# Kernel tuning notes

Measured on AMD Instinct MI355X. Metric: run time of the kernel, lower is better.

The kernel has to match this reference:

```python
import jax, jax.numpy as jnp
import numpy as np

B, S, N, C, D = 1, 6, 10000, 128, 4
HEADS, PTS = 4, 8
HF, WF = 28, 50
M = HF * WF


def setup_inputs() -> dict:
    key0 = jax.random.key(0)
    ks = jax.random.split(key0, 14)
    sc = C ** -0.5
    d = {}
    d["query"] = jax.random.normal(ks[0], (B, N, C), jnp.float32)
    d["key"] = jax.random.normal(ks[1], (S, M, B, C), jnp.float32)
    d["value"] = jax.random.normal(ks[2], (S, M, B, C), jnp.float32)
    d["query_pos"] = jax.random.normal(ks[3], (B, N, C), jnp.float32) * 0.1
    d["reference_points_cam"] = jax.random.uniform(ks[4], (S, B, N, D, 2), jnp.float32, -0.2, 1.2)
    d["bev_mask"] = jax.random.randint(ks[5], (S, B, N, D), 0, 2).astype(bool)
    d["w_off"] = jax.random.normal(ks[6], (C, HEADS * PTS * 2), jnp.float32) * sc
    d["b_off"] = jax.random.normal(ks[7], (HEADS * PTS * 2,), jnp.float32) * 0.01
    d["w_attn"] = jax.random.normal(ks[8], (C, HEADS * PTS), jnp.float32) * sc
    d["b_attn"] = jax.random.normal(ks[9], (HEADS * PTS,), jnp.float32) * 0.01
    d["w_val"] = jax.random.normal(ks[10], (C, C), jnp.float32) * sc
    d["b_val"] = jax.random.normal(ks[11], (C,), jnp.float32) * 0.01
    d["w_out"] = jax.random.normal(ks[12], (C, C), jnp.float32) * sc
    d["b_out"] = jax.random.normal(ks[13], (C,), jnp.float32) * 0.01
    d["Hf"] = HF
    d["Wf"] = WF
    return d


def reference(query, key, value, query_pos, reference_points_cam, bev_mask,
              w_off, b_off, w_attn, b_attn, w_val, b_val, w_out, b_out, Hf, Wf):
    # SpatialCrossAttention with MSDeformAttn3D (BEVFormer semantics, eval mode: dropout=identity).
    # The torch data-dependent gather/rebatch/scatter is replaced by mathematically equivalent
    # masked computation: deformable attention is per-query independent, so running it for all
    # BEV queries per camera and mask-accumulating yields identical slots.
    B_, N_, C_ = query.shape
    S_ = key.shape[0]
    D_ = reference_points_cam.shape[3]
    H, P = HEADS, PTS
    dh = C_ // H
    Pd = P // D_
    q = query + query_pos  # (B,N,C)
    off = (q @ w_off + b_off).reshape(B_, N_, H, Pd, D_, 2)
    aw = jax.nn.softmax((q @ w_attn + b_attn).reshape(B_, N_, H, P), axis=-1)  # over levels*points (L=1)
    # value projection; per-camera feature maps laid out as (B,S,H,Hf*Wf,dh)
    v = jnp.transpose(value, (2, 0, 1, 3))  # (B,S,M,C)
    v = v @ w_val + b_val
    v = v.reshape(B_, S_, Hf * Wf, H, dh).transpose(0, 1, 3, 2, 4)  # (B,S,H,M,dh)
    ref = jnp.transpose(reference_points_cam, (1, 0, 2, 3, 4))  # (B,S,N,D,2)
    norm = jnp.array([Wf, Hf], jnp.float32)  # offset_normalizer = (W, H)
    loc = ref[:, :, :, None, None, :, :] + off[:, None] / norm  # (B,S,N,H,Pd,D,2)
    loc = loc.reshape(B_, S_, N_, H, P, 2)
    # bilinear sampling, zero padding, align_corners=False
    ix = loc[..., 0] * Wf - 0.5
    iy = loc[..., 1] * Hf - 0.5
    x0 = jnp.floor(ix)
    y0 = jnp.floor(iy)

    def flat(a):  # (B,S,N,H,P) -> (B,S,H,N*P)
        return a.transpose(0, 1, 3, 2, 4).reshape(B_, S_, H, N_ * P)

    def gather(xi, yi):
        ok = (xi >= 0) & (xi < Wf) & (yi >= 0) & (yi < Hf)
        xi_c = jnp.clip(xi, 0, Wf - 1).astype(jnp.int32)
        yi_c = jnp.clip(yi, 0, Hf - 1).astype(jnp.int32)
        idx = flat(yi_c * Wf + xi_c)
        g = jnp.take_along_axis(v, idx[..., None], axis=3)  # (B,S,H,N*P,dh)
        return g * flat(ok.astype(v.dtype))[..., None]

    wx1 = ix - x0
    wy1 = iy - y0
    wx0 = 1.0 - wx1
    wy0 = 1.0 - wy1
    samp = (gather(x0, y0) * flat(wx0 * wy0)[..., None]
            + gather(x0 + 1, y0) * flat(wx1 * wy0)[..., None]
            + gather(x0, y0 + 1) * flat(wx0 * wy1)[..., None]
            + gather(x0 + 1, y0 + 1) * flat(wx1 * wy1)[..., None])  # (B,S,H,N*P,dh)
    samp = samp.reshape(B_, S_, H, N_, P, dh)
    out = jnp.einsum('bshnpd,bnhp->bsnhd', samp, aw).reshape(B_, S_, N_, C_)
    # masked scatter-accumulate back to BEV slots
    mask = jnp.transpose(jnp.any(bev_mask, axis=-1), (1, 0, 2))  # (B,S,N)
    slots = jnp.sum(out * mask[..., None].astype(out.dtype), axis=1)  # (B,N,C)
    count = jnp.maximum(mask.astype(out.dtype).sum(axis=1), 1.0)
    slots = slots / count[..., None]
    return slots @ w_out + b_out + query  # dropout is identity in eval
```

## Files before the change

### kernel.cpp

```cpp
#include <hip/hip_runtime.h>
#include <math.h>

#define S_ 6
#define N_ 10000
#define C_ 128
#define D_ 4
#define H_ 4
#define P_ 8
#define HF_ 28
#define WF_ 50
#define M_ (HF_ * WF_)
#define DH_ 32
#define SM_ (S_ * M_)
#define ABYTES (S_ * H_ * M_ * 32)
#define VB_SH (M_ * 32)
#define CQ 64
#define NCH ((N_ + CQ - 1) / CQ)

#define NB_V ((SM_ + 31) / 32)
#define NB_O ((N_ + 31) / 32)

typedef float floatx2 __attribute__((ext_vector_type(2)));

template <int NC, int MT, int MR, int MODE>
__device__ __forceinline__ void gemm_body(
    const float* __restrict__ A, const float* __restrict__ A2,
    const float* __restrict__ B0, const float* __restrict__ B1,
    const float* __restrict__ bias0, const float* __restrict__ bias1,
    float* __restrict__ outf, char* __restrict__ out8,
    int Mrows, int m0, int tid, int nthreads, float (*Alds)[132]) {
  constexpr int NTHR = (NC / 4) * (MT / MR);

  for (int i = tid; i < MT * 32; i += nthreads) {
    int r = i >> 5, k = (i & 31) * 4;
    int row = m0 + r;
    float4 v = make_float4(0.f, 0.f, 0.f, 0.f);
    if (row < Mrows) {
      v = *(const float4*)(A + (size_t)row * C_ + k);
      if (MODE == 1) {
        float4 v2 = *(const float4*)(A2 + (size_t)row * C_ + k);
        v.x += v2.x; v.y += v2.y; v.z += v2.z; v.w += v2.w;
      }
    }
    *(float4*)(&Alds[r][k]) = v;
  }
  __syncthreads();
  if (tid >= NTHR) return;

  int ci = tid % (NC / 4);
  int mi = tid / (NC / 4);
  int c0 = ci * 4, r0 = mi * MR;

  const float* bs;
  if (MODE == 1) bs = (c0 < 64) ? bias0 + c0 : bias1 + (c0 - 64);
  else bs = bias0 + c0;

  float acc[MR][4];
#pragma unroll
  for (int j = 0; j < MR; ++j)
#pragma unroll
    for (int cc = 0; cc < 4; ++cc) acc[j][cc] = bs[cc];

#pragma unroll 2
  for (int k4 = 0; k4 < C_; k4 += 4) {
    float bf[16];
#pragma unroll
    for (int kk = 0; kk < 4; ++kk) {
      int k = k4 + kk;
      float4 b4;
      if (MODE == 1)
        b4 = (c0 < 64) ? *(const float4*)(B0 + (size_t)k * 64 + c0)
                       : *(const float4*)(B1 + (size_t)k * 32 + (c0 - 64));
      else
        b4 = *(const float4*)(B0 + (size_t)k * NC + c0);
      bf[kk * 4 + 0] = b4.x; bf[kk * 4 + 1] = b4.y;
      bf[kk * 4 + 2] = b4.z; bf[kk * 4 + 3] = b4.w;
    }
    float af[MR * 4];
#pragma unroll
    for (int j = 0; j < MR; ++j) {
      float4 a4 = *(const float4*)(&Alds[r0 + j][k4]);
      af[j * 4 + 0] = a4.x; af[j * 4 + 1] = a4.y;
      af[j * 4 + 2] = a4.z; af[j * 4 + 3] = a4.w;
    }
#pragma unroll
    for (int j = 0; j < MR; ++j)
#pragma unroll
      for (int kk = 0; kk < 4; ++kk)
#pragma unroll
        for (int cc = 0; cc < 4; ++cc)
          acc[j][cc] = fmaf(af[j * 4 + kk], bf[kk * 4 + cc], acc[j][cc]);
  }

#pragma unroll
  for (int j = 0; j < MR; ++j) {
    int row = m0 + r0 + j;
    if (row >= Mrows) continue;
    if (MODE == 0) {
      int mm = row % M_;
      int h = c0 >> 5, d0 = c0 & 31;
      int s = row / M_;
      int w = __builtin_amdgcn_cvt_pk_fp8_f32(acc[j][0], acc[j][1], 0, false);
      w = __builtin_amdgcn_cvt_pk_fp8_f32(acc[j][2], acc[j][3], w, true);
      size_t hm = (size_t)s * H_ + h;
      *(int*)(out8 + (hm * M_ + mm) * 32 + d0) = w;
    } else if (MODE == 1) {
      *(float4*)(outf + (size_t)row * 96 + c0) =
          make_float4(acc[j][0], acc[j][1], acc[j][2], acc[j][3]);
    }
  }
}

__global__ __launch_bounds__(256) void prep_kernel(
    const float* __restrict__ value, const float* __restrict__ w_val,
    const float* __restrict__ b_val, char* __restrict__ vh8,
    const float* __restrict__ query, const float* __restrict__ query_pos,
    const float* __restrict__ w_off, const float* __restrict__ b_off,
    const float* __restrict__ w_attn, const float* __restrict__ b_attn,
    float* __restrict__ OFFL) {
  __shared__ float Alds[32][132];
  int bid = blockIdx.x;
  if (bid < NB_V) {
    gemm_body<128, 32, 4, 0>(value, nullptr, w_val, nullptr, b_val, nullptr,
                             nullptr, vh8, SM_, bid * 32, threadIdx.x, 256,
                             Alds);
  } else {
    gemm_body<96, 32, 4, 1>(query, query_pos, w_off, w_attn, b_off, b_attn,
                            OFFL, nullptr, N_, (bid - NB_V) * 32, threadIdx.x,
                            256, Alds);
  }
}

__global__ __launch_bounds__(512, 2) void attn4_kernel(
    const float* __restrict__ OFFL,
    const float* __restrict__ refpts,
    const int*   __restrict__ bev_mask,
    const char*  __restrict__ wsbase,
    float* __restrict__ slot) {
  __shared__ int4 Vl4[M_ * 2];

  int bid = blockIdx.x;
  int h = bid & 3;
  int q0 = (bid >> 2) * CQ;
  int tid = threadIdx.x;
  int w = tid >> 6, lane = tid & 63;
  int qg = lane >> 3, c8 = lane & 7;
  int rowsel = (c8 >> 2) & 1, xsel = (c8 >> 1) & 1, chalf = c8 & 1;

  int q = q0 + w * 8 + qg;
  int qvalid = (q < N_);
  int qc = qvalid ? q : (N_ - 1);

  float off[16];
  {
    const float* ob = OFFL + (size_t)qc * 96 + h * 16;
#pragma unroll
    for (int i = 0; i < 16; i += 4) {
      float4 t = *(const float4*)(ob + i);
      off[i] = t.x; off[i + 1] = t.y; off[i + 2] = t.z; off[i + 3] = t.w;
    }
  }
  float aw[8];
  {
    const float* lg = OFFL + (size_t)qc * 96 + 64 + h * 8;
    float mx = -1e30f;
#pragma unroll
    for (int p = 0; p < 8; ++p) { aw[p] = lg[p]; mx = fmaxf(mx, aw[p]); }
    float sum = 0.f;
#pragma unroll
    for (int p = 0; p < 8; ++p) { aw[p] = expf(aw[p] - mx); sum += aw[p]; }
    float is = 1.f / sum;
#pragma unroll
    for (int p = 0; p < 8; ++p) aw[p] *= is;
  }

  floatx2 acc[8] = {{0.f, 0.f}, {0.f, 0.f}, {0.f, 0.f}, {0.f, 0.f},
                    {0.f, 0.f}, {0.f, 0.f}, {0.f, 0.f}, {0.f, 0.f}};
  int cnt = 0;

  for (int s = 0; s < S_; ++s) {
    __syncthreads();
    {
      const int4* vsrc =
          (const int4*)(wsbase + 64 + (size_t)(s * H_ + h) * VB_SH);
      for (int i = tid; i < M_ * 2; i += 512) Vl4[i] = vsrc[i];
    }
    __syncthreads();

    const int* bm = bev_mask + ((size_t)s * N_ + qc) * D_;
    int4 bmv = *(const int4*)bm;
    int sm = (bmv.x | bmv.y | bmv.z | bmv.w) ? 1 : 0;
    cnt += sm;
    float smf = (float)sm;
    float rxy[8];
    {
      const float* rf = refpts + ((size_t)s * N_ + qc) * 8;
      float4 r0 = *(const float4*)(rf + 0);
      float4 r1 = *(const float4*)(rf + 4);
      rxy[0] = r0.x; rxy[1] = r0.y; rxy[2] = r0.z; rxy[3] = r0.w;
      rxy[4] = r1.x; rxy[5] = r1.y; rxy[6] = r1.z; rxy[7] = r1.w;
    }

#pragma unroll
    for (int p = 0; p < 8; ++p) {
      int dd = p & 3;
      float ix = rxy[dd * 2 + 0] * (float)WF_ + off[2 * p + 0] - 0.5f;
      float iy = rxy[dd * 2 + 1] * (float)HF_ + off[2 * p + 1] - 0.5f;
      float xf = floorf(ix), yf = floorf(iy);
      int x0 = (int)xf, y0 = (int)yf;
      float fx = ix - xf, fy = iy - yf;
      float wx = xsel ? fx : (1.f - fx);
      float wy = rowsel ? fy : (1.f - fy);
      int xs = x0 + xsel, ys = y0 + rowsel;
      bool ok = (xs >= 0) & (xs < WF_) & (ys >= 0) & (ys < HF_);
      float wgt = ok ? wx * wy * aw[p] * smf : 0.f;
      int xc = min(max(xs, 0), WF_ - 1);
      int yc = min(max(ys, 0), HF_ - 1);
      int vidx = (yc * WF_ + xc) * 2 + chalf;
      int4 tv = Vl4[vidx];
      floatx2 wv = {wgt, wgt};
      acc[0] += __builtin_amdgcn_cvt_pk_f32_fp8(tv.x, false) * wv;
      acc[1] += __builtin_amdgcn_cvt_pk_f32_fp8(tv.x, true)  * wv;
      acc[2] += __builtin_amdgcn_cvt_pk_f32_fp8(tv.y, false) * wv;
      acc[3] += __builtin_amdgcn_cvt_pk_f32_fp8(tv.y, true)  * wv;
      acc[4] += __builtin_amdgcn_cvt_pk_f32_fp8(tv.z, false) * wv;
      acc[5] += __builtin_amdgcn_cvt_pk_f32_fp8(tv.z, true)  * wv;
      acc[6] += __builtin_amdgcn_cvt_pk_f32_fp8(tv.w, false) * wv;
      acc[7] += __builtin_amdgcn_cvt_pk_f32_fp8(tv.w, true)  * wv;
    }
  }

  float av[16];
#pragma unroll
  for (int k = 0; k < 8; ++k) { av[2 * k] = acc[k][0]; av[2 * k + 1] = acc[k][1]; }
#pragma unroll
  for (int k = 0; k < 16; ++k) av[k] += __shfl_xor(av[k], 2);
#pragma unroll
  for (int k = 0; k < 16; ++k) av[k] += __shfl_xor(av[k], 4);

  float inv = 1.f / (float)(cnt > 0 ? cnt : 1);
  if (c8 < 2 && qvalid) {
    float* dst = slot + (size_t)q * C_ + h * DH_ + chalf * 16;
    *(float4*)(dst + 0)  = make_float4(av[0] * inv, av[1] * inv, av[2] * inv, av[3] * inv);
    *(float4*)(dst + 4)  = make_float4(av[4] * inv, av[5] * inv, av[6] * inv, av[7] * inv);
    *(float4*)(dst + 8)  = make_float4(av[8] * inv, av[9] * inv, av[10] * inv, av[11] * inv);
    *(float4*)(dst + 12) = make_float4(av[12] * inv, av[13] * inv, av[14] * inv, av[15] * inv);
  }
}

__global__ __launch_bounds__(256) void outproj_kernel(
    const float* __restrict__ slot, const float* __restrict__ query,
    const float* __restrict__ w_out, const float* __restrict__ b_out,
    float* __restrict__ out) {
  __shared__ float slds[32][132];
  int q0 = blockIdx.x * 32, tid = threadIdx.x;

  for (int i = tid; i < 32 * 32; i += 256) {
    int r = i >> 5, k = (i & 31) * 4;
    int qc = min(q0 + r, N_ - 1);
    *(float4*)(&slds[r][k]) = *(const float4*)(slot + (size_t)qc * C_ + k);
  }
  __syncthreads();

  {
    int ci = tid & 31, mi = tid >> 5;
    int c0 = ci * 4, r0 = mi * 4;
    float acc[4][4];
#pragma unroll
    for (int j = 0; j < 4; ++j) {
      int qq = min(q0 + r0 + j, N_ - 1);
      float4 qv = *(const float4*)(query + (size_t)qq * C_ + c0);
      float4 bv = *(const float4*)(b_out + c0);
      acc[j][0] = bv.x + qv.x; acc[j][1] = bv.y + qv.y;
      acc[j][2] = bv.z + qv.z; acc[j][3] = bv.w + qv.w;
    }
#pragma unroll 2
    for (int k4 = 0; k4 < C_; k4 += 4) {
      float bf[16];
#pragma unroll
      for (int kk = 0; kk < 4; ++kk) {
        float4 b4 = *(const float4*)(w_out + (size_t)(k4 + kk) * C_ + c0);
        bf[kk * 4 + 0] = b4.x; bf[kk * 4 + 1] = b4.y;
        bf[kk * 4 + 2] = b4.z; bf[kk * 4 + 3] = b4.w;
      }
      float af[16];
#pragma unroll
      for (int j = 0; j < 4; ++j) {
        float4 a4 = *(const float4*)(&slds[r0 + j][k4]);
        af[j * 4 + 0] = a4.x; af[j * 4 + 1] = a4.y;
        af[j * 4 + 2] = a4.z; af[j * 4 + 3] = a4.w;
      }
#pragma unroll
      for (int j = 0; j < 4; ++j)
#pragma unroll
        for (int kk = 0; kk < 4; ++kk)
#pragma unroll
          for (int cc = 0; cc < 4; ++cc)
            acc[j][cc] = fmaf(af[j * 4 + kk], bf[kk * 4 + cc], acc[j][cc]);
    }
#pragma unroll
    for (int j = 0; j < 4; ++j) {
      int qq = q0 + r0 + j;
      if (qq < N_)
        *(float4*)(out + (size_t)qq * C_ + c0) =
            make_float4(acc[j][0], acc[j][1], acc[j][2], acc[j][3]);
    }
  }
}

extern "C" void kernel_launch(void* const* d_in, const int* in_sizes, int n_in,
                              void* d_out, int out_size, void* d_ws, size_t ws_size,
                              hipStream_t stream) {
  const float* query     = (const float*)d_in[0];
  const float* value     = (const float*)d_in[2];
  const float* query_pos = (const float*)d_in[3];
  const float* refpts    = (const float*)d_in[4];
  const int*   bev_mask  = (const int*)d_in[5];
  const float* w_off     = (const float*)d_in[6];
  const float* b_off     = (const float*)d_in[7];
  const float* w_attn    = (const float*)d_in[8];
  const float* b_attn    = (const float*)d_in[9];
  const float* w_val     = (const float*)d_in[10];
  const float* b_val     = (const float*)d_in[11];
  const float* w_out     = (const float*)d_in[12];
  const float* b_out     = (const float*)d_in[13];

  char* ws = (char*)d_ws;
  char* vh8   = ws + 64;
  float* OFFL = (float*)(ws + 64 + 2 * (size_t)ABYTES + 64);
  float* SLOT = (float*)(ws + 64 + 2 * (size_t)ABYTES + 64 +
                         (size_t)N_ * 96 * 4);

  prep_kernel<<<NB_V + NB_O, 256, 0, stream>>>(
      value, w_val, b_val, vh8, query, query_pos, w_off, b_off, w_attn, b_attn,
      OFFL);
  attn4_kernel<<<NCH * H_, 512, 0, stream>>>(OFFL, refpts, bev_mask, ws, SLOT);
  outproj_kernel<<<(N_ + 31) / 32, 256, 0, stream>>>(SLOT, query, w_out, b_out,
                                                     (float*)d_out);
}
```

Measured before the change: 167.5 us.

## Precompute per-point bilinear params in LDS and async-load value tiles

```diff
diff --git a/kernel.cpp b/kernel.cpp
--- a/kernel.cpp
+++ b/kernel.cpp
@@ -131,93 +131,118 @@
   }
 }
 
-__global__ __launch_bounds__(512, 2) void attn4_kernel(
+__global__ __launch_bounds__(512, 4) void attn5_kernel(
     const float* __restrict__ OFFL,
     const float* __restrict__ refpts,
     const int*   __restrict__ bev_mask,
     const char*  __restrict__ wsbase,
     float* __restrict__ slot) {
   __shared__ int4 Vl4[M_ * 2];
+  __shared__ int4 Pp[CQ * 9];
 
   int bid = blockIdx.x;
   int h = bid & 3;
   int q0 = (bid >> 2) * CQ;
   int tid = threadIdx.x;
+
+  int tp = tid & 7, tq = tid >> 3;
+  int qP = q0 + tq;
+  int qPc = (qP < N_) ? qP : (N_ - 1);
+
   int w = tid >> 6, lane = tid & 63;
   int qg = lane >> 3, c8 = lane & 7;
   int rowsel = (c8 >> 2) & 1, xsel = (c8 >> 1) & 1, chalf = c8 & 1;
-
-  int q = q0 + w * 8 + qg;
-  int qvalid = (q < N_);
-  int qc = qvalid ? q : (N_ - 1);
-
-  float off[16];
+  int xsh = xsel << 4;
+  int ql = w * 8 + qg;
+  int qG = q0 + ql;
+  int qGvalid = (qG < N_);
+
+  float aw_p, offx, offy;
   {
-    const float* ob = OFFL + (size_t)qc * 96 + h * 16;
-#pragma unroll
-    for (int i = 0; i < 16; i += 4) {
-      float4 t = *(const float4*)(ob + i);
-      off[i] = t.x; off[i + 1] = t.y; off[i + 2] = t.z; off[i + 3] = t.w;
-    }
-  }
-  float aw[8];
-  {
-    const float* lg = OFFL + (size_t)qc * 96 + 64 + h * 8;
+    const float* lg = OFFL + (size_t)qPc * 96 + 64 + h * 8;
+    float4 l0 = *(const float4*)(lg + 0);
+    float4 l1 = *(const float4*)(lg + 4);
+    float e[8] = {l0.x, l0.y, l0.z, l0.w, l1.x, l1.y, l1.z, l1.w};
     float mx = -1e30f;
 #pragma unroll
-    for (int p = 0; p < 8; ++p) { aw[p] = lg[p]; mx = fmaxf(mx, aw[p]); }
+    for (int p = 0; p < 8; ++p) mx = fmaxf(mx, e[p]);
     float sum = 0.f;
 #pragma unroll
-    for (int p = 0; p < 8; ++p) { aw[p] = expf(aw[p] - mx); sum += aw[p]; }
-    float is = 1.f / sum;
-#pragma unroll
-    for (int p = 0; p < 8; ++p) aw[p] *= is;
+    for (int p = 0; p < 8; ++p) { e[p] = expf(e[p] - mx); sum += e[p]; }
+    aw_p = e[tp] / sum;
+    int pd = tp >> 2, dd = tp & 3;
+    const float* ob = OFFL + (size_t)qPc * 96 + h * 16 + pd * 8 + dd * 2;
+    offx = ob[0]; offy = ob[1];
   }
 
   floatx2 acc[8] = {{0.f, 0.f}, {0.f, 0.f}, {0.f, 0.f}, {0.f, 0.f},
                     {0.f, 0.f}, {0.f, 0.f}, {0.f, 0.f}, {0.f, 0.f}};
-  int cnt = 0;
 
   for (int s = 0; s < S_; ++s) {
     __syncthreads();
+
     {
-      const int4* vsrc =
-          (const int4*)(wsbase + 64 + (size_t)(s * H_ + h) * VB_SH);
-      for (int i = tid; i < M_ * 2; i += 512) Vl4[i] = vsrc[i];
-    }
-    __syncthreads();
-
-    const int* bm = bev_mask + ((size_t)s * N_ + qc) * D_;
-    int4 bmv = *(const int4*)bm;
-    int sm = (bmv.x | bmv.y | bmv.z | bmv.w) ? 1 : 0;
-    cnt += sm;
-    float smf = (float)sm;
-    float rxy[8];
+      const char* gsrc = wsbase + 64 + (size_t)(s * H_ + h) * VB_SH;
+#pragma unroll
+      for (int r = 0; r < 6; ++r) {
+        int i = r * 512 + tid;
+        if (i < M_ * 2) {
+          __builtin_amdgcn_global_load_lds(
+              (const __attribute__((address_space(1))) unsigned int*)(gsrc +
+                                                                      i * 16),
+              (__attribute__((address_space(3))) unsigned int*)&Vl4[i], 16, 0,
+              0);
+        }
+      }
+    }
+
     {
-      const float* rf = refpts + ((size_t)s * N_ + qc) * 8;
-      float4 r0 = *(const float4*)(rf + 0);
-      float4 r1 = *(const float4*)(rf + 4);
-      rxy[0] = r0.x; rxy[1] = r0.y; rxy[2] = r0.z; rxy[3] = r0.w;
-      rxy[4] = r1.x; rxy[5] = r1.y; rxy[6] = r1.z; rxy[7] = r1.w;
-    }
-
-#pragma unroll
-    for (int p = 0; p < 8; ++p) {
-      int dd = p & 3;
-      float ix = rxy[dd * 2 + 0] * (float)WF_ + off[2 * p + 0] - 0.5f;
-      float iy = rxy[dd * 2 + 1] * (float)HF_ + off[2 * p + 1] - 0.5f;
+      int dd = tp & 3;
+      const float* rf = refpts + ((size_t)s * N_ + qPc) * 8 + dd * 2;
+      float rx = rf[0], ry = rf[1];
+      const int* bm = bev_mask + ((size_t)s * N_ + qPc) * D_;
+      int4 bmv = *(const int4*)bm;
+      float A = ((bmv.x | bmv.y | bmv.z | bmv.w) ? 1.f : 0.f) * aw_p;
+      float ix = rx * (float)WF_ + offx - 0.5f;
+      float iy = ry * (float)HF_ + offy - 0.5f;
       float xf = floorf(ix), yf = floorf(iy);
       int x0 = (int)xf, y0 = (int)yf;
       float fx = ix - xf, fy = iy - yf;
-      float wx = xsel ? fx : (1.f - fx);
-      float wy = rowsel ? fy : (1.f - fy);
-      int xs = x0 + xsel, ys = y0 + rowsel;
-      bool ok = (xs >= 0) & (xs < WF_) & (ys >= 0) & (ys < HF_);
-      float wgt = ok ? wx * wy * aw[p] * smf : 0.f;
-      int xc = min(max(xs, 0), WF_ - 1);
-      int yc = min(max(ys, 0), HF_ - 1);
-      int vidx = (yc * WF_ + xc) * 2 + chalf;
-      int4 tv = Vl4[vidx];
+      float gx = 1.f - fx, gy = 1.f - fy;
+      bool vx0 = (x0 >= 0) && (x0 < WF_);
+      bool vx1 = (x0 >= -1) && (x0 < WF_ - 1);
+      bool vy0 = (y0 >= 0) && (y0 < HF_);
+      bool vy1 = (y0 >= -1) && (y0 < HF_ - 1);
+      float w00 = (vx0 && vy0) ? gx * gy * A : 0.f;
+      float w10 = (vx1 && vy0) ? fx * gy * A : 0.f;
+      float w01 = (vx0 && vy1) ? gx * fy * A : 0.f;
+      float w11 = (vx1 && vy1) ? fx * fy * A : 0.f;
+      int yt = min(max(y0, 0), HF_ - 1) * WF_;
+      int yb = min(max(y0 + 1, 0), HF_ - 1) * WF_;
+      int xc0 = min(max(x0, 0), WF_ - 1);
+      int xc1 = min(max(x0 + 1, 0), WF_ - 1);
+      int4 pk;
+      pk.x = ((yt + xc0) * 2) | (((yt + xc1) * 2) << 16);
+      pk.y = ((yb + xc0) * 2) | (((yb + xc1) * 2) << 16);
+      union { _Float16 hf[2]; int iv; } u01, u23;
+      u01.hf[0] = (_Float16)w00; u01.hf[1] = (_Float16)w10;
+      u23.hf[0] = (_Float16)w01; u23.hf[1] = (_Float16)w11;
+      pk.z = u01.iv;
+      pk.w = u23.iv;
+      Pp[tq * 9 + tp] = pk;
+    }
+    __syncthreads();
+
+#pragma unroll
+    for (int p = 0; p < 8; ++p) {
+      int4 prm = Pp[ql * 9 + p];
+      int vword = rowsel ? prm.y : prm.x;
+      int vidx = (int)(((unsigned)vword >> xsh) & 0xffffu);
+      int wword = rowsel ? prm.w : prm.z;
+      union { unsigned short u; _Float16 hf; } cu;
+      cu.u = (unsigned short)((unsigned)wword >> xsh);
+      float wgt = (float)cu.hf;
+      int4 tv = Vl4[vidx + chalf];
       floatx2 wv = {wgt, wgt};
       acc[0] += __builtin_amdgcn_cvt_pk_f32_fp8(tv.x, false) * wv;
       acc[1] += __builtin_amdgcn_cvt_pk_f32_fp8(tv.x, true)  * wv;
@@ -238,9 +263,16 @@
 #pragma unroll
   for (int k = 0; k < 16; ++k) av[k] += __shfl_xor(av[k], 4);
 
-  float inv = 1.f / (float)(cnt > 0 ? cnt : 1);
-  if (c8 < 2 && qvalid) {
-    float* dst = slot + (size_t)q * C_ + h * DH_ + chalf * 16;
+  if (c8 < 2 && qGvalid) {
+    int cnt = 0;
+#pragma unroll
+    for (int s = 0; s < S_; ++s) {
+      const int* bm = bev_mask + ((size_t)s * N_ + qG) * D_;
+      int4 bmv = *(const int4*)bm;
+      cnt += (bmv.x | bmv.y | bmv.z | bmv.w) ? 1 : 0;
+    }
+    float inv = 1.f / (float)(cnt > 0 ? cnt : 1);
+    float* dst = slot + (size_t)qG * C_ + h * DH_ + chalf * 16;
     *(float4*)(dst + 0)  = make_float4(av[0] * inv, av[1] * inv, av[2] * inv, av[3] * inv);
     *(float4*)(dst + 4)  = make_float4(av[4] * inv, av[5] * inv, av[6] * inv, av[7] * inv);
     *(float4*)(dst + 8)  = make_float4(av[8] * inv, av[9] * inv, av[10] * inv, av[11] * inv);
@@ -334,7 +366,7 @@
   prep_kernel<<<NB_V + NB_O, 256, 0, stream>>>(
       value, w_val, b_val, vh8, query, query_pos, w_off, b_off, w_attn, b_attn,
       OFFL);
-  attn4_kernel<<<NCH * H_, 512, 0, stream>>>(OFFL, refpts, bev_mask, ws, SLOT);
+  attn5_kernel<<<NCH * H_, 512, 0, stream>>>(OFFL, refpts, bev_mask, ws, SLOT);
   outproj_kernel<<<(N_ + 31) / 32, 256, 0, stream>>>(SLOT, query, w_out, b_out,
                                                      (float*)d_out);
 }
```

After: 158.3 us. 5.5% less time.
